# Kernel tuning notes

Hardware: AMD Instinct MI355X
Metric: run time of the kernel (lower is better)

## Reference

```python
import jax, jax.numpy as jnp
import numpy as np

KNN_K = 30  # args.knn_k; top_k keeps knn_k + 1 entries per row
EPS = 1e-12  # torch F.normalize clamp_min eps


def setup_inputs() -> dict:
    key = jax.random.key(0)
    ks = jax.random.split(key, 4)
    N, F, H, O = 12288, 768, 512, 256

    def lin(k, out_d, in_d):
        return jax.random.normal(k, (out_d, in_d), jnp.float32) * (1.0 / np.sqrt(in_d))

    return {
        "features": jax.random.normal(ks[0], (N, F), jnp.float32),
        "W1": lin(ks[1], H, F), "b1": jnp.zeros((H,), jnp.float32),
        "W2": lin(ks[2], H, H), "b2": jnp.zeros((H,), jnp.float32),
        "W3": lin(ks[3], O, H), "b3": jnp.zeros((O,), jnp.float32),
    }


def reference(features, W1, b1, W2, b2, W3, b3):
    # MLP: relu on all but last layer
    x = jax.nn.relu(features @ W1.T + b1)
    x = jax.nn.relu(x @ W2.T + b2)
    x = x @ W3.T + b3
    # L2 normalize rows (torch F.normalize, p=2, dim=1)
    e = x / jnp.maximum(jnp.linalg.norm(x, axis=1, keepdims=True), EPS)
    # full pairwise cosine similarity [N, N]
    sim = e @ e.T
    # per-row top-(k+1) sparsification: keep values at top positions, zero rest
    _, idx = jax.lax.top_k(sim, KNN_K + 1)  # [N, k+1]
    N = sim.shape[0]
    mask = jnp.zeros_like(sim).at[jnp.arange(N)[:, None], idx].set(1.0)
    return jax.nn.relu(sim * mask)
```

## Files before the change

### kernel.cpp

```cpp
#include <hip/hip_runtime.h>
#include <cstdint>
#include <cstddef>

#define NROWS 12288
#define FDIM 768
#define HDIM 512
#define ODIM 256
#define TOPK 31
#define CAP 1536

template<bool RELU>
__global__ __launch_bounds__(256)
void gemm_nt_serial(const float* __restrict__ A, const float* __restrict__ B,
                    const float* __restrict__ bias, float* __restrict__ C,
                    int Nout, int K)
{
  __shared__ float As[32][68];
  __shared__ float Bs[32][68];
  const int tid = threadIdx.x;
  const int tx = tid & 15, ty = tid >> 4;
  const int r0 = blockIdx.y * 64, c0 = blockIdx.x * 64;
  float acc[4][4] = {};
  float accC[4][4];
  bool first = true;
  const int Khalf = K / 2;

  for (int k0 = 0; k0 < K; k0 += 32) {
#pragma unroll
    for (int l = 0; l < 2; ++l) {
      const int lin = l * 256 + tid;
      const int row = lin >> 3, kq = lin & 7;
      const float4 a = *(const float4*)(A + (size_t)(r0 + row) * K + k0 + kq * 4);
      As[kq + 0][row] = a.x; As[kq + 8][row] = a.y;
      As[kq + 16][row] = a.z; As[kq + 24][row] = a.w;
      const float4 b = *(const float4*)(B + (size_t)(c0 + row) * K + k0 + kq * 4);
      Bs[kq + 0][row] = b.x; Bs[kq + 8][row] = b.y;
      Bs[kq + 16][row] = b.z; Bs[kq + 24][row] = b.w;
    }
    __syncthreads();
#pragma unroll
    for (int kk = 0; kk < 32; ++kk) {
      const int kp = ((kk & 3) << 3) | (kk >> 2);
      const float4 av = *(const float4*)&As[kp][ty * 4];
      const float4 bv = *(const float4*)&Bs[kp][tx * 4];
      const float a4[4] = {av.x, av.y, av.z, av.w};
      const float b4[4] = {bv.x, bv.y, bv.z, bv.w};
#pragma unroll
      for (int i = 0; i < 4; ++i)
#pragma unroll
        for (int j = 0; j < 4; ++j)
          acc[i][j] = fmaf(a4[i], b4[j], acc[i][j]);
    }
    __syncthreads();

    if ((k0 + 32 == Khalf) || (k0 + 32 == K)) {
#pragma unroll
      for (int i = 0; i < 4; ++i)
#pragma unroll
        for (int j = 0; j < 4; ++j) {
          accC[i][j] = first ? acc[i][j] : __fadd_rn(accC[i][j], acc[i][j]);
          acc[i][j] = 0.f;
        }
      first = false;
    }
  }

  const float4 bq = *(const float4*)(bias + c0 + tx * 4);
  const float bb[4] = {bq.x, bq.y, bq.z, bq.w};
#pragma unroll
  for (int i = 0; i < 4; ++i) {
    float v[4];
#pragma unroll
    for (int j = 0; j < 4; ++j) {
      v[j] = __fadd_rn(accC[i][j], bb[j]);
      if (RELU) v[j] = fmaxf(v[j], 0.f);
    }
    float4 o; o.x = v[0]; o.y = v[1]; o.z = v[2]; o.w = v[3];
    *(float4*)(C + (size_t)(r0 + ty * 4 + i) * Nout + c0 + tx * 4) = o;
  }
}

template<bool RELU>
__global__ __launch_bounds__(256)
void gemm_big_nt(const float* __restrict__ A, const float* __restrict__ B,
                 const float* __restrict__ bias, float* __restrict__ C,
                 int Nout, int K)
{
  __shared__ float As[32][132];
  __shared__ float Bs[32][132];
  const int tid = threadIdx.x;
  const int tx = tid & 15, ty = tid >> 4;
  const int r0 = blockIdx.y * 128, c0 = blockIdx.x * 128;
  float acc[8][8] = {};
  float accC[8][8];
  bool first = true;
  const int Khalf = K / 2;

  for (int k0 = 0; k0 < K; k0 += 32) {
#pragma unroll
    for (int l = 0; l < 4; ++l) {
      const int lin = l * 256 + tid;
      const int row = lin >> 3, q = lin & 7;
      const float4 a = *(const float4*)(A + (size_t)(r0 + row) * K + k0 + q * 4);
      As[q + 0][row] = a.x; As[q + 8][row] = a.y;
      As[q + 16][row] = a.z; As[q + 24][row] = a.w;
      const float4 b = *(const float4*)(B + (size_t)(c0 + row) * K + k0 + q * 4);
      Bs[q + 0][row] = b.x; Bs[q + 8][row] = b.y;
      Bs[q + 16][row] = b.z; Bs[q + 24][row] = b.w;
    }
    __syncthreads();
#pragma unroll
    for (int kk = 0; kk < 32; ++kk) {
      const int kp = ((kk & 3) << 3) | (kk >> 2);
      float a8[8], b8[8];
      *(float4*)&a8[0] = *(const float4*)&As[kp][ty * 8];
      *(float4*)&a8[4] = *(const float4*)&As[kp][ty * 8 + 4];
      *(float4*)&b8[0] = *(const float4*)&Bs[kp][tx * 4];
      *(float4*)&b8[4] = *(const float4*)&Bs[kp][64 + tx * 4];
#pragma unroll
      for (int i = 0; i < 8; ++i)
#pragma unroll
        for (int j = 0; j < 8; ++j)
          acc[i][j] = fmaf(a8[i], b8[j], acc[i][j]);
    }
    __syncthreads();

    if ((k0 + 32 == Khalf) || (k0 + 32 == K)) {
#pragma unroll
      for (int i = 0; i < 8; ++i)
#pragma unroll
        for (int j = 0; j < 8; ++j) {
          accC[i][j] = first ? acc[i][j] : __fadd_rn(accC[i][j], acc[i][j]);
          acc[i][j] = 0.f;
        }
      first = false;
    }
  }

  const float4 bq0 = *(const float4*)(bias + c0 + tx * 4);
  const float4 bq1 = *(const float4*)(bias + c0 + 64 + tx * 4);
  const float bb[8] = {bq0.x, bq0.y, bq0.z, bq0.w, bq1.x, bq1.y, bq1.z, bq1.w};
#pragma unroll
  for (int i = 0; i < 8; ++i) {
    float v[8];
#pragma unroll
    for (int j = 0; j < 8; ++j) {
      v[j] = __fadd_rn(accC[i][j], bb[j]);
      if (RELU) v[j] = fmaxf(v[j], 0.f);
    }
    float* dst = C + (size_t)(r0 + ty * 8 + i) * Nout + c0;
    float4 o0; o0.x = v[0]; o0.y = v[1]; o0.z = v[2]; o0.w = v[3];
    float4 o1; o1.x = v[4]; o1.y = v[5]; o1.z = v[6]; o1.w = v[7];
    *(float4*)(dst + tx * 4) = o0;
    *(float4*)(dst + 64 + tx * 4) = o1;
  }
}

__global__ __launch_bounds__(64)
void l2norm_np(float* __restrict__ X)
{
  const int row = blockIdx.x * 64 + threadIdx.x;
  float* x = X + (size_t)row * ODIM;

  float S = 0.f;
#pragma unroll
  for (int h = 0; h < 2; ++h) {
    const float* a = x + h * 128;
    float r0 = __fmul_rn(a[0], a[0]);
    float r1 = __fmul_rn(a[1], a[1]);
    float r2 = __fmul_rn(a[2], a[2]);
    float r3 = __fmul_rn(a[3], a[3]);
    float r4 = __fmul_rn(a[4], a[4]);
    float r5 = __fmul_rn(a[5], a[5]);
    float r6 = __fmul_rn(a[6], a[6]);
    float r7 = __fmul_rn(a[7], a[7]);
    for (int i = 8; i < 128; i += 8) {
      r0 = __fadd_rn(r0, __fmul_rn(a[i + 0], a[i + 0]));
      r1 = __fadd_rn(r1, __fmul_rn(a[i + 1], a[i + 1]));
      r2 = __fadd_rn(r2, __fmul_rn(a[i + 2], a[i + 2]));
      r3 = __fadd_rn(r3, __fmul_rn(a[i + 3], a[i + 3]));
      r4 = __fadd_rn(r4, __fmul_rn(a[i + 4], a[i + 4]));
      r5 = __fadd_rn(r5, __fmul_rn(a[i + 5], a[i + 5]));
      r6 = __fadd_rn(r6, __fmul_rn(a[i + 6], a[i + 6]));
      r7 = __fadd_rn(r7, __fmul_rn(a[i + 7], a[i + 7]));
    }
    const float half = __fadd_rn(
        __fadd_rn(__fadd_rn(r0, r1), __fadd_rn(r2, r3)),
        __fadd_rn(__fadd_rn(r4, r5), __fadd_rn(r6, r7)));
    S = (h == 0) ? half : __fadd_rn(S, half);
  }

  const float d = fmaxf(__fsqrt_rn(S), 1e-12f);
  for (int k = 0; k < ODIM; ++k) x[k] = __fdiv_rn(x[k], d);
}

__global__ __launch_bounds__(256)
void sim_gemm_sym(const float* __restrict__ E, float* __restrict__ S)
{
  __shared__ float As[32][132];
  __shared__ float Bs[32][132];
  const int tid = threadIdx.x;
  const int bx = blockIdx.x, by = blockIdx.y;
  if (bx < by) return;
  const int tx = tid & 15, ty = tid >> 4;
  const int r0 = by * 128, c0 = bx * 128;
  float acc[8][8] = {};

#pragma unroll
  for (int k0 = 0; k0 < ODIM; k0 += 32) {
#pragma unroll
    for (int l = 0; l < 4; ++l) {
      const int lin = l * 256 + tid;
      const int row = lin >> 3, q = lin & 7;
      const float4 a = *(const float4*)(E + (size_t)(r0 + row) * ODIM + k0 + q * 4);
      As[q + 0][row] = a.x; As[q + 8][row] = a.y;
      As[q + 16][row] = a.z; As[q + 24][row] = a.w;
      const float4 b = *(const float4*)(E + (size_t)(c0 + row) * ODIM + k0 + q * 4);
      Bs[q + 0][row] = b.x; Bs[q + 8][row] = b.y;
      Bs[q + 16][row] = b.z; Bs[q + 24][row] = b.w;
    }
    __syncthreads();
#pragma unroll
    for (int kk = 0; kk < 32; ++kk) {
      const int kp = ((kk & 3) << 3) | (kk >> 2);
      float a8[8], b8[8];
      *(float4*)&a8[0] = *(const float4*)&As[kp][ty * 8];
      *(float4*)&a8[4] = *(const float4*)&As[kp][ty * 8 + 4];
      *(float4*)&b8[0] = *(const float4*)&Bs[kp][tx * 4];
      *(float4*)&b8[4] = *(const float4*)&Bs[kp][64 + tx * 4];
#pragma unroll
      for (int i = 0; i < 8; ++i)
#pragma unroll
        for (int j = 0; j < 8; ++j)
          acc[i][j] = fmaf(a8[i], b8[j], acc[i][j]);
    }
    __syncthreads();
  }

#pragma unroll
  for (int i = 0; i < 8; ++i) {
    float4 o0, o1;
    o0.x = acc[i][0]; o0.y = acc[i][1]; o0.z = acc[i][2]; o0.w = acc[i][3];
    o1.x = acc[i][4]; o1.y = acc[i][5]; o1.z = acc[i][6]; o1.w = acc[i][7];
    float* dst = S + (size_t)(r0 + ty * 8 + i) * NROWS + c0;
    *(float4*)(dst + tx * 4) = o0;
    *(float4*)(dst + 64 + tx * 4) = o1;
  }

  if (bx == by) return;

#pragma unroll
  for (int h = 0; h < 2; ++h)
#pragma unroll
    for (int j = 0; j < 4; ++j) {
      const int col = c0 + h * 64 + tx * 4 + j;
      float4 a, b;
      a.x = acc[0][h * 4 + j]; a.y = acc[1][h * 4 + j];
      a.z = acc[2][h * 4 + j]; a.w = acc[3][h * 4 + j];
      b.x = acc[4][h * 4 + j]; b.y = acc[5][h * 4 + j];
      b.z = acc[6][h * 4 + j]; b.w = acc[7][h * 4 + j];
      float* dst = S + (size_t)col * NROWS + r0 + ty * 8;
      *(float4*)dst = a;
      *(float4*)(dst + 4) = b;
    }
}

__device__ __forceinline__ uint32_t tokey(float f)
{
  const uint32_t u = __float_as_uint(f);
  return (u & 0x80000000u) ? ~u : (u | 0x80000000u);
}

__device__ __forceinline__ float relu_fromkey(uint32_t k)
{
  return (k > 0x80000000u) ? __uint_as_float(k & 0x7FFFFFFFu) : 0.f;
}

__device__ __forceinline__ uint64_t packkc(uint32_t key, uint32_t col)
{
  return ((uint64_t)key << 32) | (0xFFFFFFFFu - col);
}

__global__ __launch_bounds__(256)
void topk_mask(float* __restrict__ S)
{
  __shared__ uint64_t c0s[256];
  __shared__ uint64_t cand[CAP];
  __shared__ uint64_t wlist[TOPK];
  __shared__ uint64_t Lsh;
  __shared__ int cnt_sh, pos_sh;

  const int tid = threadIdx.x;
  const int row = blockIdx.x;
  float* Srow = S + (size_t)row * NROWS;

  uint4 kq[12];
  uint64_t c0 = 0;
#pragma unroll
  for (int i = 0; i < 12; ++i) {
    const float4 f = *(const float4*)(Srow + tid * 4 + i * 1024);
    const uint32_t cb = tid * 4 + i * 1024;
    uint4 k;
    k.x = tokey(f.x); k.y = tokey(f.y); k.z = tokey(f.z); k.w = tokey(f.w);
    kq[i] = k;
    uint64_t p;
    p = packkc(k.x, cb + 0); if (p > c0) c0 = p;
    p = packkc(k.y, cb + 1); if (p > c0) c0 = p;
    p = packkc(k.z, cb + 2); if (p > c0) c0 = p;
    p = packkc(k.w, cb + 3); if (p > c0) c0 = p;
  }
  c0s[tid] = c0;
  if (tid == 0) cnt_sh = 0;
  __syncthreads();

  int rank = 0;
  for (int j = 0; j < 256; ++j) rank += (c0s[j] > c0) ? 1 : 0;
  if (rank == TOPK - 1) Lsh = c0;
  __syncthreads();
  uint64_t L = Lsh;

  int my = 0;
#pragma unroll
  for (int i = 0; i < 12; ++i) {
    const uint32_t cb = tid * 4 + i * 1024;
    my += (packkc(kq[i].x, cb + 0) >= L) ? 1 : 0;
    my += (packkc(kq[i].y, cb + 1) >= L) ? 1 : 0;
    my += (packkc(kq[i].z, cb + 2) >= L) ? 1 : 0;
    my += (packkc(kq[i].w, cb + 3) >= L) ? 1 : 0;
  }
  atomicAdd(&cnt_sh, my);
  __syncthreads();
  int C = cnt_sh;

  uint64_t hi = 0xFFFFFFFFFFFFFFFFull;
  while (C > CAP) {
    const uint64_t mid = L + ((hi - L) >> 1);
    if (tid == 0) cnt_sh = 0;
    __syncthreads();
    int m2 = 0;
#pragma unroll
    for (int i = 0; i < 12; ++i) {
      const uint32_t cb = tid * 4 + i * 1024;
      m2 += (packkc(kq[i].x, cb + 0) >= mid) ? 1 : 0;
      m2 += (packkc(kq[i].y, cb + 1) >= mid) ? 1 : 0;
      m2 += (packkc(kq[i].z, cb + 2) >= mid) ? 1 : 0;
      m2 += (packkc(kq[i].w, cb + 3) >= mid) ? 1 : 0;
    }
    atomicAdd(&cnt_sh, m2);
    __syncthreads();
    const int c2 = cnt_sh;
    if (c2 >= TOPK) { L = mid; C = c2; my = m2; } else { hi = mid; }
    __syncthreads();
  }

  if (tid == 0) pos_sh = 0;
  __syncthreads();
  int base = (my > 0) ? atomicAdd(&pos_sh, my) : 0;
#pragma unroll
  for (int i = 0; i < 12; ++i) {
    const uint32_t cb = tid * 4 + i * 1024;
    uint64_t p;
    p = packkc(kq[i].x, cb + 0); if (p >= L) cand[base++] = p;
    p = packkc(kq[i].y, cb + 1); if (p >= L) cand[base++] = p;
    p = packkc(kq[i].z, cb + 2); if (p >= L) cand[base++] = p;
    p = packkc(kq[i].w, cb + 3); if (p >= L) cand[base++] = p;
  }
  __syncthreads();

  for (int idx = tid; idx < C; idx += 256) {
    const uint64_t p = cand[idx];
    int r = 0;
    for (int j = 0; j < C; ++j) r += (cand[j] > p) ? 1 : 0;
    if (r < TOPK) wlist[r] = p;
  }

  const float4 z = {0.f, 0.f, 0.f, 0.f};
#pragma unroll
  for (int i = 0; i < 12; ++i)
    *(float4*)(Srow + tid * 4 + i * 1024) = z;
  __syncthreads();
  if (tid < TOPK) {
    const uint64_t p = wlist[tid];
    const uint32_t col = 0xFFFFFFFFu - (uint32_t)p;
    Srow[col] = relu_fromkey((uint32_t)(p >> 32));
  }
}

extern "C" void kernel_launch(void* const* d_in, const int* in_sizes, int n_in,
                              void* d_out, int out_size, void* d_ws, size_t ws_size,
                              hipStream_t stream)
{
  const float* feat = (const float*)d_in[0];
  const float* W1 = (const float*)d_in[1];
  const float* b1 = (const float*)d_in[2];
  const float* W2 = (const float*)d_in[3];
  const float* b2 = (const float*)d_in[4];
  const float* W3 = (const float*)d_in[5];
  const float* b3 = (const float*)d_in[6];
  float* S = (float*)d_out;

  float* X1 = (float*)d_ws;
  float* X2 = X1 + (size_t)NROWS * HDIM;
  float* E  = X2 + (size_t)NROWS * HDIM;

  gemm_big_nt<true><<<dim3(HDIM / 128, NROWS / 128), 256, 0, stream>>>(
      feat, W1, b1, X1, HDIM, FDIM);
  gemm_big_nt<true><<<dim3(HDIM / 128, NROWS / 128), 256, 0, stream>>>(
      X1, W2, b2, X2, HDIM, HDIM);
  gemm_nt_serial<false><<<dim3(ODIM / 64, NROWS / 64), 256, 0, stream>>>(
      X2, W3, b3, E, ODIM, HDIM);
  l2norm_np<<<NROWS / 64, 64, 0, stream>>>(E);
  sim_gemm_sym<<<dim3(NROWS / 128, NROWS / 128), 256, 0, stream>>>(E, S);
  topk_mask<<<NROWS, 256, 0, stream>>>(S);
}
```

Before: 1.091 ms.

## Prefetch next K-tile into registers and compact symmetric similarity grid

In the MLP GEMM and the symmetric similarity GEMM, the next 32-wide K slice of A and B is now loaded into registers while the current slice is being multiplied out of shared memory. This overlaps global-load latency with the FMA loop. The similarity kernel also switches from a full 96x96 grid, where half the blocks exit at once, to a 49x96 grid that maps each block to a pair of tiles by a cyclic offset. That removes the idle launches. The offset-48 tiles are computed twice with identical writes, and holding the prefetched data in registers raises register pressure.

```diff
diff --git a/kernel.cpp b/kernel.cpp
--- a/kernel.cpp
+++ b/kernel.cpp
@@ -90,25 +90,37 @@
   __shared__ float Bs[32][132];
   const int tid = threadIdx.x;
   const int tx = tid & 15, ty = tid >> 4;
+  const int q = tid & 7, rbase = tid >> 3;
   const int r0 = blockIdx.y * 128, c0 = blockIdx.x * 128;
   float acc[8][8] = {};
   float accC[8][8];
   bool first = true;
   const int Khalf = K / 2;
 
+  float4 ra[4], rb[4];
+#pragma unroll
+  for (int l = 0; l < 4; ++l) {
+    ra[l] = *(const float4*)(A + (size_t)(r0 + l * 32 + rbase) * K + q * 4);
+    rb[l] = *(const float4*)(B + (size_t)(c0 + l * 32 + rbase) * K + q * 4);
+  }
+
   for (int k0 = 0; k0 < K; k0 += 32) {
 #pragma unroll
     for (int l = 0; l < 4; ++l) {
-      const int lin = l * 256 + tid;
-      const int row = lin >> 3, q = lin & 7;
-      const float4 a = *(const float4*)(A + (size_t)(r0 + row) * K + k0 + q * 4);
-      As[q + 0][row] = a.x; As[q + 8][row] = a.y;
-      As[q + 16][row] = a.z; As[q + 24][row] = a.w;
-      const float4 b = *(const float4*)(B + (size_t)(c0 + row) * K + k0 + q * 4);
-      Bs[q + 0][row] = b.x; Bs[q + 8][row] = b.y;
-      Bs[q + 16][row] = b.z; Bs[q + 24][row] = b.w;
-    }
-    __syncthreads();
+      const int row = l * 32 + rbase;
+      As[q + 0][row] = ra[l].x; As[q + 8][row] = ra[l].y;
+      As[q + 16][row] = ra[l].z; As[q + 24][row] = ra[l].w;
+      Bs[q + 0][row] = rb[l].x; Bs[q + 8][row] = rb[l].y;
+      Bs[q + 16][row] = rb[l].z; Bs[q + 24][row] = rb[l].w;
+    }
+    __syncthreads();
+    if (k0 + 32 < K) {
+#pragma unroll
+      for (int l = 0; l < 4; ++l) {
+        ra[l] = *(const float4*)(A + (size_t)(r0 + l * 32 + rbase) * K + k0 + 32 + q * 4);
+        rb[l] = *(const float4*)(B + (size_t)(c0 + l * 32 + rbase) * K + k0 + 32 + q * 4);
+      }
+    }
 #pragma unroll
     for (int kk = 0; kk < 32; ++kk) {
       const int kp = ((kk & 3) << 3) | (kk >> 2);
@@ -200,26 +212,40 @@
   __shared__ float As[32][132];
   __shared__ float Bs[32][132];
   const int tid = threadIdx.x;
-  const int bx = blockIdx.x, by = blockIdx.y;
-  if (bx < by) return;
+  const int a0 = blockIdx.y;
+  int b0 = a0 + blockIdx.x;
+  if (b0 >= NROWS / 128) b0 -= NROWS / 128;
+  const int by = min(a0, b0), bx = max(a0, b0);
   const int tx = tid & 15, ty = tid >> 4;
+  const int q = tid & 7, rbase = tid >> 3;
   const int r0 = by * 128, c0 = bx * 128;
   float acc[8][8] = {};
 
+  float4 ra[4], rb[4];
+#pragma unroll
+  for (int l = 0; l < 4; ++l) {
+    ra[l] = *(const float4*)(E + (size_t)(r0 + l * 32 + rbase) * ODIM + q * 4);
+    rb[l] = *(const float4*)(E + (size_t)(c0 + l * 32 + rbase) * ODIM + q * 4);
+  }
+
 #pragma unroll
   for (int k0 = 0; k0 < ODIM; k0 += 32) {
 #pragma unroll
     for (int l = 0; l < 4; ++l) {
-      const int lin = l * 256 + tid;
-      const int row = lin >> 3, q = lin & 7;
-      const float4 a = *(const float4*)(E + (size_t)(r0 + row) * ODIM + k0 + q * 4);
-      As[q + 0][row] = a.x; As[q + 8][row] = a.y;
-      As[q + 16][row] = a.z; As[q + 24][row] = a.w;
-      const float4 b = *(const float4*)(E + (size_t)(c0 + row) * ODIM + k0 + q * 4);
-      Bs[q + 0][row] = b.x; Bs[q + 8][row] = b.y;
-      Bs[q + 16][row] = b.z; Bs[q + 24][row] = b.w;
-    }
-    __syncthreads();
+      const int row = l * 32 + rbase;
+      As[q + 0][row] = ra[l].x; As[q + 8][row] = ra[l].y;
+      As[q + 16][row] = ra[l].z; As[q + 24][row] = ra[l].w;
+      Bs[q + 0][row] = rb[l].x; Bs[q + 8][row] = rb[l].y;
+      Bs[q + 16][row] = rb[l].z; Bs[q + 24][row] = rb[l].w;
+    }
+    __syncthreads();
+    if (k0 + 32 < ODIM) {
+#pragma unroll
+      for (int l = 0; l < 4; ++l) {
+        ra[l] = *(const float4*)(E + (size_t)(r0 + l * 32 + rbase) * ODIM + k0 + 32 + q * 4);
+        rb[l] = *(const float4*)(E + (size_t)(c0 + l * 32 + rbase) * ODIM + k0 + 32 + q * 4);
+      }
+    }
 #pragma unroll
     for (int kk = 0; kk < 32; ++kk) {
       const int kp = ((kk & 3) << 3) | (kk >> 2);
@@ -254,14 +280,14 @@
 #pragma unroll
     for (int j = 0; j < 4; ++j) {
       const int col = c0 + h * 64 + tx * 4 + j;
-      float4 a, b;
-      a.x = acc[0][h * 4 + j]; a.y = acc[1][h * 4 + j];
-      a.z = acc[2][h * 4 + j]; a.w = acc[3][h * 4 + j];
-      b.x = acc[4][h * 4 + j]; b.y = acc[5][h * 4 + j];
-      b.z = acc[6][h * 4 + j]; b.w = acc[7][h * 4 + j];
+      float4 va, vb;
+      va.x = acc[0][h * 4 + j]; va.y = acc[1][h * 4 + j];
+      va.z = acc[2][h * 4 + j]; va.w = acc[3][h * 4 + j];
+      vb.x = acc[4][h * 4 + j]; vb.y = acc[5][h * 4 + j];
+      vb.z = acc[6][h * 4 + j]; vb.w = acc[7][h * 4 + j];
       float* dst = S + (size_t)col * NROWS + r0 + ty * 8;
-      *(float4*)dst = a;
-      *(float4*)(dst + 4) = b;
+      *(float4*)dst = va;
+      *(float4*)(dst + 4) = vb;
     }
 }
 
@@ -410,6 +436,6 @@
   gemm_nt_serial<false><<<dim3(ODIM / 64, NROWS / 64), 256, 0, stream>>>(
       X2, W3, b3, E, ODIM, HDIM);
   l2norm_np<<<NROWS / 64, 64, 0, stream>>>(E);
-  sim_gemm_sym<<<dim3(NROWS / 128, NROWS / 128), 256, 0, stream>>>(E, S);
+  sim_gemm_sym<<<dim3(49, NROWS / 128), 256, 0, stream>>>(E, S);
   topk_mask<<<NROWS, 256, 0, stream>>>(S);
 }
```

Result: slower. 1.320 ms (+21.0%).
